# Kernel tuning notes

Measured on AMD Instinct MI355X. Metric: run time of the kernel, lower is better.

Reference implementation:

```python
import jax, jax.numpy as jnp
import numpy as np

N = 13627
E = 504378
D = 500


def _seg_softmax(e, seg, n):
    m = jax.ops.segment_max(e, seg, num_segments=n)
    ex = jnp.exp(e - m[seg])
    s = jax.ops.segment_sum(ex, seg, num_segments=n)
    return ex / (s[seg] + 1e-16)


def _gatv2(x, src, dst, Wl, Wr, att, b, n):
    # PyG GATv2Conv (heads=1): message = Wl x_src; score uses Wl x_src + Wr x_dst
    xl = x @ Wl                                   # [N, F]
    xr = x @ Wr                                   # [N, F]
    e = jax.nn.leaky_relu(xl[src] + xr[dst], 0.2) @ att   # [E]
    a = _seg_softmax(e, dst, n)                   # segment softmax over targets
    out = jax.ops.segment_sum(a[:, None] * xl[src], dst, num_segments=n)
    return out + b


def setup_inputs() -> dict:
    key = jax.random.key(0)
    ks = jax.random.split(key, 24)
    s = 0.05
    inp = {
        'x': jax.random.normal(ks[0], (N, D), dtype=jnp.float32),
        'edge_index': jax.random.randint(ks[1], (2, E), 0, N),
        'neg_edge_index': jax.random.randint(ks[2], (2, E), 0, N),
        'Wl1': jax.random.normal(ks[3], (D, 300)) * s,
        'Wr1': jax.random.normal(ks[4], (D, 300)) * s,
        'att1': jax.random.normal(ks[5], (300,)) * s,
        'b1': jnp.zeros((300,)),
        'Wl2': jax.random.normal(ks[6], (300, 100)) * s,
        'Wr2': jax.random.normal(ks[7], (300, 100)) * s,
        'att2': jax.random.normal(ks[8], (100,)) * s,
        'b2': jnp.zeros((100,)),
        'Wl3': jax.random.normal(ks[9], (100, 1)) * s,
        'Wr3': jax.random.normal(ks[10], (100, 1)) * s,
        'att3': jax.random.normal(ks[11], (1,)) * s,
        'b3': jnp.zeros((1,)),
        'W_lin1': jax.random.normal(ks[12], (D, 100)) * s,
        'b_lin1': jnp.zeros((100,)),
        'W_lin2': jax.random.normal(ks[13], (D, 100)) * s,
        'b_lin2': jnp.zeros((100,)),
        'c1': jnp.array([0.5], dtype=jnp.float32),
        'c2': jnp.array([0.5], dtype=jnp.float32),
    }
    return inp


def reference(x, edge_index, neg_edge_index, Wl1, Wr1, att1, b1, Wl2, Wr2, att2, b2,
              Wl3, Wr3, att3, b3, W_lin1, b_lin1, W_lin2, b_lin2, c1, c2):
    # eval mode: dropout / dropout_adj are identity
    loops = jnp.arange(N)
    src = jnp.concatenate([edge_index[0], loops])   # GATv2Conv adds self loops
    dst = jnp.concatenate([edge_index[1], loops])

    h1 = jax.nn.relu(_gatv2(x, src, dst, Wl1, Wr1, att1, b1, N))
    h2 = jax.nn.relu(_gatv2(h1, src, dst, Wl2, Wr2, att2, b2, N))

    xo = h2 + jax.nn.relu(x @ W_lin1 + b_lin1)
    z = h2 + jax.nn.relu(x @ W_lin2 + b_lin2)

    # link-prediction reconstruction loss
    pos_s = jnp.sum(z[edge_index[0]] * z[edge_index[1]], axis=1)
    pos_loss = -jnp.mean(jnp.log(jax.nn.sigmoid(pos_s) + 1e-15))
    neg_s = jnp.sum(z[neg_edge_index[0]] * z[neg_edge_index[1]], axis=1)
    neg_loss = -jnp.mean(jnp.log(1.0 - jax.nn.sigmoid(neg_s) + 1e-15))
    r_loss = pos_loss + neg_loss

    out = _gatv2(xo, src, dst, Wl3, Wr3, att3, b3, N)   # [N, 1]
    return out, r_loss, c1, c2
```

## Files before the change

kernel.cpp:

```cpp
#include <hip/hip_runtime.h>
#include <hip/hip_bf16.h>

#define NODES 13627
#define DIM   500

typedef short short8 __attribute__((ext_vector_type(8)));
typedef float f32x4 __attribute__((ext_vector_type(4)));
typedef float floatx2 __attribute__((ext_vector_type(2)));

__device__ inline float wave_reduce_sum(float v) {
#pragma unroll
    for (int o = 32; o > 0; o >>= 1) v += __shfl_xor(v, o, 64);
    return v;
}

__device__ inline void store_v(float* p, float v) { *p = v; }
__device__ inline void store_v(__hip_bfloat16* p, float v) { *p = __float2bfloat16(v); }

__device__ inline float blo(unsigned w) { unsigned t = w << 16;        return __builtin_bit_cast(float, t); }
__device__ inline float bhi(unsigned w) { unsigned t = w & 0xffff0000u; return __builtin_bit_cast(float, t); }

__device__ inline unsigned char to_fp8(float v) {
    int r = __builtin_amdgcn_cvt_pk_fp8_f32(v, v, 0, false);
    return (unsigned char)(r & 0xff);
}

__device__ inline unsigned pk2bf(float a, float b) {
    unsigned la = (unsigned)__builtin_bit_cast(unsigned short, __float2bfloat16(a));
    unsigned hb = (unsigned)__builtin_bit_cast(unsigned short, __float2bfloat16(b));
    return la | (hb << 16);
}

struct b4 { __hip_bfloat16 a, b, c, d; };

__global__ __launch_bounds__(256) void hist_kernel(const int* __restrict__ dst,
                                                   int* __restrict__ cnt, int E) {
    int i = blockIdx.x * blockDim.x + threadIdx.x;
    if (i < E) atomicAdd(&cnt[dst[i]], 1);
}

__global__ __launch_bounds__(1024) void scan_kernel(int* __restrict__ cnt_cur,
                                                    int* __restrict__ off, int n) {
    __shared__ int wsum[16];
    const int tid = threadIdx.x, lane = tid & 63, w = tid >> 6;
    int carry = 0;
    for (int base = 0; base < n; base += 1024) {
        int i = base + tid;
        int v = (i < n) ? cnt_cur[i] : 0;
        int s = v;
#pragma unroll
        for (int o = 1; o < 64; o <<= 1) {
            int t = __shfl_up(s, o, 64);
            if (lane >= o) s += t;
        }
        if (lane == 63) wsum[w] = s;
        __syncthreads();
        if (w == 0 && lane < 16) {
            int x = wsum[lane];
            int sx = x;
#pragma unroll
            for (int o = 1; o < 16; o <<= 1) {
                int t = __shfl_up(sx, o, 64);
                if (lane >= o) sx += t;
            }
            wsum[lane] = sx;
        }
        __syncthreads();
        int wo = (w == 0) ? 0 : wsum[w - 1];
        int total = wsum[15];
        int excl = carry + wo + (s - v);
        if (i < n) { off[i] = excl; cnt_cur[i] = excl; }
        carry += total;
        __syncthreads();
    }
    if (tid == 0) off[n] = carry;
}

__global__ __launch_bounds__(256) void scatter_kernel(const int* __restrict__ src,
                                                      const int* __restrict__ dst,
                                                      int* __restrict__ cur,
                                                      int* __restrict__ ssrc, int E) {
    int i = blockIdx.x * blockDim.x + threadIdx.x;
    if (i < E) {
        int p = atomicAdd(&cur[dst[i]], 1);
        ssrc[p] = src[i];
    }
}

__global__ __launch_bounds__(256) void convert_all_kernel(
    const float* __restrict__ x,
    const float* __restrict__ Wl1, const float* __restrict__ Wr1,
    const float* __restrict__ Wl2, const float* __restrict__ Wr2,
    const float* __restrict__ Ws1, const float* __restrict__ Ws2,
    const float* __restrict__ bs1, const float* __restrict__ bs2,
    __hip_bfloat16* __restrict__ W1T, __hip_bfloat16* __restrict__ W2T,
    __hip_bfloat16* __restrict__ WsT, float* __restrict__ bcat,
    __hip_bfloat16* __restrict__ xb, int M) {
    int i = blockIdx.x * 256 + threadIdx.x;
    if (i < 327680) {
        int n = i >> 9, k = i & 511;
        float v = 0.f;
        if (k < 500) {
            if (n < 300) v = Wl1[k * 300 + n];
            else if (n < 600) v = Wr1[k * 300 + n - 300];
        }
        W1T[i] = __float2bfloat16(v);
    } else if (i < 409600) {
        int j = i - 327680;
        int n = j / 320, k = j - n * 320;
        float v = 0.f;
        if (k < 300) {
            if (n < 100) v = Wl2[k * 100 + n];
            else if (n < 200) v = Wr2[k * 100 + n - 100];
        }
        W2T[j] = __float2bfloat16(v);
    } else if (i < 540672) {
        int j = i - 409600;
        int n = j >> 9, k = j & 511;
        float v = 0.f;
        if (k < 500) {
            if (n < 100) v = Ws1[k * 100 + n];
            else if (n < 200) v = Ws2[k * 100 + n - 100];
        }
        WsT[j] = __float2bfloat16(v);
    } else if (i < 540928) {
        int n = i - 540672;
        float v = 0.f;
        if (n < 100) v = bs1[n];
        else if (n < 200) v = bs2[n - 100];
        bcat[n] = v;
    } else {
        int j = i - 540928;
        if (j >= M * 128) return;
        int m = j >> 7, k = (j & 127) << 2;
        b4 o;
        if (k < 500) {
            float4 v = *(const float4*)(x + (size_t)m * 500 + k);
            o.a = __float2bfloat16(v.x); o.b = __float2bfloat16(v.y);
            o.c = __float2bfloat16(v.z); o.d = __float2bfloat16(v.w);
        } else {
            o.a = o.b = o.c = o.d = __float2bfloat16(0.f);
        }
        *(b4*)(xb + (size_t)m * 512 + k) = o;
    }
}

template <int EPI, typename TC>
__global__ __launch_bounds__(256) void mfma_gemm(
    const __hip_bfloat16* __restrict__ A, const __hip_bfloat16* __restrict__ BT,
    TC* __restrict__ C, const float* __restrict__ bias, const float* __restrict__ h2,
    unsigned char* __restrict__ p8, __hip_bfloat16* __restrict__ pb,
    int M, int Kp, int Nn, int ldc) {
    __shared__ short AsF[8 * 64 * 8];
    __shared__ short BsF[4 * 64 * 8];
    const int t = threadIdx.x;
    const int w = t >> 6, lane = t & 63;
    const int c = t & 3, rr = t >> 2;
    const int m0 = blockIdx.y * 128, n0 = blockIdx.x * 64;

    f32x4 acc[2][4];
#pragma unroll
    for (int i = 0; i < 2; i++)
#pragma unroll
        for (int j = 0; j < 4; j++) acc[i][j] = (f32x4){0.f, 0.f, 0.f, 0.f};

    for (int k0 = 0; k0 < Kp; k0 += 32) {
#pragma unroll
        for (int r = 0; r < 2; r++) {
            int m = r * 64 + rr;
            int gm = m0 + m; if (gm >= M) gm = M - 1;
            float4 v = *(const float4*)(A + (size_t)gm * Kp + k0 + c * 8);
            int mi = m >> 4, sl = m & 15;
            *(float4*)(&AsF[(mi * 64 + c * 16 + sl) * 8]) = v;
        }
        {
            int n = rr;
            float4 v = *(const float4*)(BT + (size_t)(n0 + n) * Kp + k0 + c * 8);
            int ni = n >> 4, sl = n & 15;
            *(float4*)(&BsF[(ni * 64 + c * 16 + sl) * 8]) = v;
        }
        __syncthreads();
        short8 a0 = *(const short8*)(&AsF[((w * 2 + 0) * 64 + lane) * 8]);
        short8 a1 = *(const short8*)(&AsF[((w * 2 + 1) * 64 + lane) * 8]);
#pragma unroll
        for (int j = 0; j < 4; j++) {
            short8 b = *(const short8*)(&BsF[(j * 64 + lane) * 8]);
            acc[0][j] = __builtin_amdgcn_mfma_f32_16x16x32_bf16(a0, b, acc[0][j], 0, 0, 0);
            acc[1][j] = __builtin_amdgcn_mfma_f32_16x16x32_bf16(a1, b, acc[1][j], 0, 0, 0);
        }
        __syncthreads();
    }

    const int q = lane >> 4, sl = lane & 15;
#pragma unroll
    for (int i = 0; i < 2; i++) {
#pragma unroll
        for (int j = 0; j < 4; j++) {
#pragma unroll
            for (int reg = 0; reg < 4; reg++) {
                int gm = m0 + w * 32 + i * 16 + q * 4 + reg;
                int gn = n0 + j * 16 + sl;
                if (gm >= M) continue;
                float v = acc[i][j][reg];
                if constexpr (EPI == 1) {
                    if (gn < 300)       p8[(size_t)gm * 304 + gn] = to_fp8(v);
                    else if (gn < 600)  pb[(size_t)gm * 320 + (gn - 300)] = __float2bfloat16(v);
                    else if (gn < 620)  pb[(size_t)gm * 320 + (gn - 300)] = __float2bfloat16(0.f);
                    else if (gn < 624)  p8[(size_t)gm * 304 + (gn - 320)] = 0;
                } else if constexpr (EPI == 2) {
                    if (gn < 100)       p8[(size_t)gm * 112 + gn] = to_fp8(v);
                    else if (gn < 200)  pb[(size_t)gm * 128 + (gn - 100)] = __float2bfloat16(v);
                    else if (gn < 212)  p8[(size_t)gm * 112 + (gn - 100)] = 0;
                    else if (gn < 240)  pb[(size_t)gm * 128 + (gn - 112)] = __float2bfloat16(0.f);
                } else if constexpr (EPI == 3) {
                    if (gn < 200) {
                        int cn = gn < 100 ? gn : gn - 100;
                        float val = fmaxf(v + bias[gn], 0.f) + h2[(size_t)gm * 100 + cn];
                        if (gn < 100) C[(size_t)gm * 100 + gn] = val;
                        else p8[(size_t)gm * 128 + (gn - 100)] = to_fp8(val);
                    } else if (gn < 228) {
                        p8[(size_t)gm * 128 + (gn - 100)] = 0;
                    }
                } else {
                    store_v(&C[(size_t)gm * ldc + gn], v);
                }
            }
        }
    }
}

template <int F, int NJ, int SL8, int SRB, int SOUT, int JSL, typename TOUT>
__global__ __launch_bounds__(256) void gat_f8_kernel(
    const unsigned char* __restrict__ xl8, const __hip_bfloat16* __restrict__ xrb,
    const float* __restrict__ att, const float* __restrict__ bias,
    const int* __restrict__ off, const int* __restrict__ ssrc,
    TOUT* __restrict__ out, int n) {
    __shared__ float sden[2];
    __shared__ float sacc[2][NJ * 64];
    const int t = threadIdx.x;
    const int lane = t & 63;
    const int sl = lane & 15, q = lane >> 4;
    const int half = (t >> 6) & 1;
    const int pairIdx = t >> 7;
    int wid = blockIdx.x * 2 + pairIdx;
    if (wid >= n) wid = n - 1;

    float attv[NJ * 4], xrv[NJ * 4], acc[NJ * 4];
    const unsigned* xru = (const unsigned*)xrb + (size_t)wid * (SRB / 2);
#pragma unroll
    for (int j = 0; j < NJ; j++) {
        const int f0 = sl * 4 + j * 64;
        if (f0 < F) {
            float4 a4 = *(const float4*)(att + f0);
            attv[j * 4 + 0] = a4.x; attv[j * 4 + 1] = a4.y;
            attv[j * 4 + 2] = a4.z; attv[j * 4 + 3] = a4.w;
        } else {
            attv[j * 4 + 0] = attv[j * 4 + 1] = attv[j * 4 + 2] = attv[j * 4 + 3] = 0.f;
        }
        unsigned u0 = __builtin_nontemporal_load(xru + (f0 >> 1));
        unsigned u1 = __builtin_nontemporal_load(xru + (f0 >> 1) + 1);
        xrv[j * 4 + 0] = blo(u0); xrv[j * 4 + 1] = bhi(u0);
        xrv[j * 4 + 2] = blo(u1); xrv[j * 4 + 3] = bhi(u1);
        acc[j * 4 + 0] = acc[j * 4 + 1] = acc[j * 4 + 2] = acc[j * 4 + 3] = 0.f;
    }

    const int s0 = off[wid], s1 = off[wid + 1];
    const int h0 = (s1 - s0) >> 1;
    const int eb = half ? (s0 + h0) : (s0 - 1);
    const int ee = half ? s1 : (s0 + h0);
    float den = 0.f;

    for (int e0 = eb; e0 < ee; e0 += 8) {
        const int eA = e0 + q, eB = e0 + 4 + q;
        const bool actA = eA < ee, actB = eB < ee;
        int srcA = wid, srcB = wid;
        if (actA && eA >= s0) srcA = __builtin_nontemporal_load(ssrc + eA);
        if (actB && eB >= s0) srcB = __builtin_nontemporal_load(ssrc + eB);
        const unsigned char* rowA = xl8 + (size_t)srcA * SL8;
        const unsigned char* rowB = xl8 + (size_t)srcB * SL8;
        unsigned uA[NJ], uB[NJ];
#pragma unroll
        for (int j = 0; j < NJ; j++) {
            const bool ld = (j < NJ - 1) || (sl < JSL);
            const int offb = sl * 4 + j * 64;
            uA[j] = ld ? *(const unsigned*)(rowA + offb) : 0u;
            uB[j] = ld ? *(const unsigned*)(rowB + offb) : 0u;
        }
        float xlvA[NJ * 4], xlvB[NJ * 4];
        float pA = 0.f, pB = 0.f;
#pragma unroll
        for (int j = 0; j < NJ; j++) {
            floatx2 loA = __builtin_amdgcn_cvt_pk_f32_fp8((int)uA[j], false);
            floatx2 hiA = __builtin_amdgcn_cvt_pk_f32_fp8((int)uA[j], true);
            floatx2 loB = __builtin_amdgcn_cvt_pk_f32_fp8((int)uB[j], false);
            floatx2 hiB = __builtin_amdgcn_cvt_pk_f32_fp8((int)uB[j], true);
            float vA[4] = {loA.x, loA.y, hiA.x, hiA.y};
            float vB[4] = {loB.x, loB.y, hiB.x, hiB.y};
#pragma unroll
            for (int cc = 0; cc < 4; cc++) {
                xlvA[j * 4 + cc] = vA[cc];
                xlvB[j * 4 + cc] = vB[cc];
                float tA = vA[cc] + xrv[j * 4 + cc];
                float tB = vB[cc] + xrv[j * 4 + cc];
                pA += attv[j * 4 + cc] * fmaxf(tA, 0.2f * tA);
                pB += attv[j * 4 + cc] * fmaxf(tB, 0.2f * tB);
            }
        }
        pA += __shfl_xor(pA, 1, 64);  pB += __shfl_xor(pB, 1, 64);
        pA += __shfl_xor(pA, 2, 64);  pB += __shfl_xor(pB, 2, 64);
        pA += __shfl_xor(pA, 4, 64);  pB += __shfl_xor(pB, 4, 64);
        pA += __shfl_xor(pA, 8, 64);  pB += __shfl_xor(pB, 8, 64);
        float exA = actA ? expf(pA) : 0.f;
        float exB = actB ? expf(pB) : 0.f;
        den += exA + exB;
#pragma unroll
        for (int i = 0; i < NJ * 4; i++) acc[i] += exA * xlvA[i] + exB * xlvB[i];
    }

#pragma unroll
    for (int o = 16; o <= 32; o <<= 1) {
        den += __shfl_xor(den, o, 64);
#pragma unroll
        for (int i = 0; i < NJ * 4; i++) acc[i] += __shfl_xor(acc[i], o, 64);
    }

    if (half == 1 && lane < 16) {
        if (lane == 0) sden[pairIdx] = den;
#pragma unroll
        for (int j = 0; j < NJ; j++)
            *(float4*)(&sacc[pairIdx][sl * 4 + j * 64]) =
                make_float4(acc[j * 4 + 0], acc[j * 4 + 1], acc[j * 4 + 2], acc[j * 4 + 3]);
    }
    __syncthreads();
    if (half == 0 && lane < 16) {
        den += sden[pairIdx];
        const float inv = 1.f / (den + 1e-16f);
#pragma unroll
        for (int j = 0; j < NJ; j++) {
            const int f0 = sl * 4 + j * 64;
            if (f0 >= SOUT) continue;
            float4 o4 = *(float4*)(&sacc[pairIdx][f0]);
            float vv[4] = {acc[j * 4 + 0] + o4.x, acc[j * 4 + 1] + o4.y,
                           acc[j * 4 + 2] + o4.z, acc[j * 4 + 3] + o4.w};
            float r[4];
#pragma unroll
            for (int cc = 0; cc < 4; cc++) {
                const int f = f0 + cc;
                float v = 0.f;
                if (f < F) v = fmaxf(vv[cc] * inv + bias[f], 0.f);
                r[cc] = v;
            }
            if constexpr (sizeof(TOUT) == 4) {
                float* op = (float*)out + (size_t)wid * SOUT + f0;
                __builtin_nontemporal_store(r[0], op + 0);
                __builtin_nontemporal_store(r[1], op + 1);
                __builtin_nontemporal_store(r[2], op + 2);
                __builtin_nontemporal_store(r[3], op + 3);
            } else {
                unsigned* op = (unsigned*)out + (size_t)wid * (SOUT / 2) + (f0 >> 1);
                __builtin_nontemporal_store(pk2bf(r[0], r[1]), op);
                __builtin_nontemporal_store(pk2bf(r[2], r[3]), op + 1);
            }
        }
    }
}

__global__ __launch_bounds__(256) void gemm_vec1_kernel(
    const float* __restrict__ xo, const float* __restrict__ wl,
    const float* __restrict__ wr, float* __restrict__ xl3,
    float* __restrict__ xr3, int M, int ldx) {
    const int wid = blockIdx.x * 4 + (threadIdx.x >> 6);
    const int lane = threadIdx.x & 63;
    if (wid >= M) return;
    float a = 0.f, b = 0.f;
    for (int f = lane; f < 100; f += 64) {
        float v = xo[(size_t)wid * ldx + f];
        a += v * wl[f];
        b += v * wr[f];
    }
    a = wave_reduce_sum(a);
    b = wave_reduce_sum(b);
    if (lane == 0) { xl3[wid] = a; xr3[wid] = b; }
}

__global__ __launch_bounds__(256) void gat3_kernel(
    const float* __restrict__ xl3, const float* __restrict__ xr3,
    const float* __restrict__ att3, const float* __restrict__ b3,
    const int* __restrict__ off, const int* __restrict__ ssrc,
    float* __restrict__ out, int n) {
    const int wid = blockIdx.x * 4 + (threadIdx.x >> 6);
    const int lane = threadIdx.x & 63;
    if (wid >= n) return;
    const float xrv = xr3[wid];
    const float att = att3[0];
    float num = 0.f, den = 0.f;
    const int s0 = off[wid], s1 = off[wid + 1];
    for (int e = s0 - 1 + lane; e < s1; e += 64) {
        int src = (e < s0) ? wid : ssrc[e];
        float xlv = xl3[src];
        float t = xlv + xrv;
        float g = t > 0.f ? t : 0.2f * t;
        float ex = expf(g * att);
        den += ex;
        num += ex * xlv;
    }
    num = wave_reduce_sum(num);
    den = wave_reduce_sum(den);
    if (lane == 0) out[wid] = num / (den + 1e-16f) + b3[0];
}

__global__ __launch_bounds__(256) void loss_kernel(
    const unsigned char* __restrict__ z8, const int* __restrict__ pos,
    const int* __restrict__ neg, float* __restrict__ part, int nb, int E) {
    const int lane = threadIdx.x & 63;
    const int sl = lane & 15;
    const int wlocal = threadIdx.x >> 6;
    const int q = lane >> 4;
    const int nq = gridDim.x * 16;
    const int qid = (blockIdx.x * 4 + wlocal) * 4 + q;
    const int total = 2 * E;
    float psum = 0.f, nsum = 0.f;

    for (int base = qid; base < total; base += 4 * nq) {
        uint2 au[4], bu[4];
        bool act[4], isN[4];
#pragma unroll
        for (int s = 0; s < 4; s++) {
            int it = base + s * nq;
            act[s] = it < total;
            int itc = act[s] ? it : 0;
            isN[s] = itc >= E;
            int e = isN[s] ? itc - E : itc;
            const int* ei = isN[s] ? neg : pos;
            int u = ei[e], v = ei[E + e];
            au[s] = *(const uint2*)(z8 + (size_t)u * 128 + sl * 8);
            bu[s] = *(const uint2*)(z8 + (size_t)v * 128 + sl * 8);
        }
#pragma unroll
        for (int s = 0; s < 4; s++) {
            floatx2 a0 = __builtin_amdgcn_cvt_pk_f32_fp8((int)au[s].x, false);
            floatx2 a1 = __builtin_amdgcn_cvt_pk_f32_fp8((int)au[s].x, true);
            floatx2 a2 = __builtin_amdgcn_cvt_pk_f32_fp8((int)au[s].y, false);
            floatx2 a3 = __builtin_amdgcn_cvt_pk_f32_fp8((int)au[s].y, true);
            floatx2 b0 = __builtin_amdgcn_cvt_pk_f32_fp8((int)bu[s].x, false);
            floatx2 b1 = __builtin_amdgcn_cvt_pk_f32_fp8((int)bu[s].x, true);
            floatx2 b2 = __builtin_amdgcn_cvt_pk_f32_fp8((int)bu[s].y, false);
            floatx2 b3 = __builtin_amdgcn_cvt_pk_f32_fp8((int)bu[s].y, true);
            float p = a0.x * b0.x + a0.y * b0.y + a1.x * b1.x + a1.y * b1.y
                    + a2.x * b2.x + a2.y * b2.y + a3.x * b3.x + a3.y * b3.y;
            p += __shfl_xor(p, 1, 64);
            p += __shfl_xor(p, 2, 64);
            p += __shfl_xor(p, 4, 64);
            p += __shfl_xor(p, 8, 64);
            if (sl == 0 && act[s]) {
                float sig = 1.f / (1.f + expf(-p));
                if (isN[s]) nsum += logf(1.f - sig + 1e-15f);
                else        psum += logf(sig + 1e-15f);
            }
        }
    }
    float pw = wave_reduce_sum(psum);
    float nw = wave_reduce_sum(nsum);
    __shared__ float sp[4], sn[4];
    if (lane == 0) { sp[wlocal] = pw; sn[wlocal] = nw; }
    __syncthreads();
    if (threadIdx.x == 0) {
        part[blockIdx.x]      = sp[0] + sp[1] + sp[2] + sp[3];
        part[nb + blockIdx.x] = sn[0] + sn[1] + sn[2] + sn[3];
    }
}

__global__ __launch_bounds__(1024) void finalize_kernel(
    const float* __restrict__ part, int nb,
    const float* __restrict__ c1, const float* __restrict__ c2,
    float* __restrict__ out, int n, int E) {
    __shared__ float sp[16], sn[16];
    const int tid = threadIdx.x, lane = tid & 63, w = tid >> 6;
    float p = 0.f, q = 0.f;
    for (int i = tid; i < nb; i += 1024) { p += part[i]; q += part[nb + i]; }
    p = wave_reduce_sum(p);
    q = wave_reduce_sum(q);
    if (lane == 0) { sp[w] = p; sn[w] = q; }
    __syncthreads();
    if (tid == 0) {
        float tp = 0.f, tq = 0.f;
#pragma unroll
        for (int i = 0; i < 16; i++) { tp += sp[i]; tq += sn[i]; }
        out[n]     = -(tp + tq) / (float)E;
        out[n + 1] = c1[0];
        out[n + 2] = c2[0];
    }
}

extern "C" void kernel_launch(void* const* d_in, const int* in_sizes, int n_in,
                              void* d_out, int out_size, void* d_ws, size_t ws_size,
                              hipStream_t stream) {
    const float* x      = (const float*)d_in[0];
    const int*   ei     = (const int*)d_in[1];
    const int*   nei    = (const int*)d_in[2];
    const float* Wl1    = (const float*)d_in[3];
    const float* Wr1    = (const float*)d_in[4];
    const float* att1   = (const float*)d_in[5];
    const float* b1     = (const float*)d_in[6];
    const float* Wl2    = (const float*)d_in[7];
    const float* Wr2    = (const float*)d_in[8];
    const float* att2   = (const float*)d_in[9];
    const float* b2     = (const float*)d_in[10];
    const float* Wl3    = (const float*)d_in[11];
    const float* Wr3    = (const float*)d_in[12];
    const float* att3   = (const float*)d_in[13];
    const float* b3     = (const float*)d_in[14];
    const float* Wlin1  = (const float*)d_in[15];
    const float* blin1  = (const float*)d_in[16];
    const float* Wlin2  = (const float*)d_in[17];
    const float* blin2  = (const float*)d_in[18];
    const float* c1     = (const float*)d_in[19];
    const float* c2     = (const float*)d_in[20];
    float* out = (float*)d_out;

    const int E = in_sizes[1] / 2;
    const int N = NODES;
    const int LOSS_BLOCKS = 4096;

    char* ws = (char*)d_ws;
    unsigned char*  xl8  = (unsigned char*)(ws + 0);
    unsigned char*  xl28 = (unsigned char*)(ws + 0);
    __hip_bfloat16* xrb  = (__hip_bfloat16*)(ws + 4194304);
    __hip_bfloat16* xr2b = (__hip_bfloat16*)(ws + 4194304);
    float*          xo   = (float*)(ws + 4194304);
    unsigned char*  z8   = (unsigned char*)(ws + 9645312);
    __hip_bfloat16* h1b  = (__hip_bfloat16*)(ws + 12915712);
    float*          h2   = (float*)(ws + 12915712);
    __hip_bfloat16* xb   = (__hip_bfloat16*)(ws + 21637120);
    __hip_bfloat16* W1T  = (__hip_bfloat16*)(ws + 35591168);
    __hip_bfloat16* W2T  = (__hip_bfloat16*)(ws + 36246528);
    __hip_bfloat16* WsT  = (__hip_bfloat16*)(ws + 36410368);
    float*          bcat = (float*)(ws + 36672512);
    float*          xl3  = (float*)(ws + 36673536);
    float*          xr3  = (float*)(ws + 36728064);
    int*            ioff = (int*)(ws + 36782592);
    int*            cur  = (int*)(ws + 36837376);
    int*            ssrc = (int*)(ws + 36892160);
    float*          part = (float*)(ws + 38909952);

    hipMemsetAsync(cur, 0, sizeof(int) * N, stream);

    hist_kernel<<<(E + 255) / 256, 256, 0, stream>>>(ei + E, cur, E);
    scan_kernel<<<1, 1024, 0, stream>>>(cur, ioff, N);
    scatter_kernel<<<(E + 255) / 256, 256, 0, stream>>>(ei, ei + E, cur, ssrc, E);

    convert_all_kernel<<<(540928 + N * 128 + 255) / 256, 256, 0, stream>>>(
        x, Wl1, Wr1, Wl2, Wr2, Wlin1, Wlin2, blin1, blin2,
        W1T, W2T, WsT, bcat, xb, N);

    mfma_gemm<1, __hip_bfloat16><<<dim3(10, 107), 256, 0, stream>>>(
        xb, W1T, (__hip_bfloat16*)nullptr, nullptr, nullptr, xl8, xrb, N, 512, 640, 0);
    gat_f8_kernel<300, 5, 304, 320, 320, 11, __hip_bfloat16>
        <<<(N + 1) / 2, 256, 0, stream>>>(xl8, xrb, att1, b1, ioff, ssrc, h1b, N);

    mfma_gemm<2, __hip_bfloat16><<<dim3(4, 107), 256, 0, stream>>>(
        h1b, W2T, (__hip_bfloat16*)nullptr, nullptr, nullptr, xl28, xr2b, N, 320, 256, 0);
    gat_f8_kernel<100, 2, 112, 128, 100, 9, float>
        <<<(N + 1) / 2, 256, 0, stream>>>(xl28, xr2b, att2, b2, ioff, ssrc, h2, N);

    mfma_gemm<3, float><<<dim3(4, 107), 256, 0, stream>>>(
        xb, WsT, xo, bcat, h2, z8, nullptr, N, 512, 256, 0);

    loss_kernel<<<LOSS_BLOCKS, 256, 0, stream>>>(z8, ei, nei, part, LOSS_BLOCKS, E);

    gemm_vec1_kernel<<<(N + 3) / 4, 256, 0, stream>>>(xo, Wl3, Wr3, xl3, xr3, N, 100);
    gat3_kernel<<<(N + 3) / 4, 256, 0, stream>>>(xl3, xr3, att3, b3, ioff, ssrc, out, N);

    finalize_kernel<<<1, 1024, 0, stream>>>(part, LOSS_BLOCKS, c1, c2, out, N, E);
}
```

Baseline: 403.4 us.

## Decompose leaky-ReLU attention score into per-node dots plus abs term

Rewrites leaky_relu(s) as 0.6*s + 0.4*|s|, so the linear part of the attention score becomes per-node dot products att·xl and att·xr. A new kernel precomputes these once per node, leaving only an fma with fabs per feature in the edge loop. The GAT edge loop also drops from two edges per iteration to one, which lowers register pressure at the cost of less memory-level parallelism per iteration. It adds an extra kernel launch and small per-node arrays, and the algebraic split slightly changes floating-point rounding.

After: 408.3 us. About the same (+1.2%).

```diff
diff --git a/kernel.cpp b/kernel.cpp
--- a/kernel.cpp
+++ b/kernel.cpp
@@ -229,10 +229,34 @@
     }
 }
 
+template <int F, int SL8, int SRB>
+__global__ __launch_bounds__(256) void attdot_kernel(
+    const unsigned char* __restrict__ xl8, const __hip_bfloat16* __restrict__ xrb,
+    const float* __restrict__ att, float* __restrict__ sxl, float* __restrict__ sxr,
+    int n) {
+    const int wid = blockIdx.x * 4 + (threadIdx.x >> 6);
+    const int lane = threadIdx.x & 63;
+    if (wid >= n) return;
+    float al = 0.f, ar = 0.f;
+    for (int f0 = lane * 4; f0 < F; f0 += 256) {
+        float4 a = *(const float4*)(att + f0);
+        unsigned u = *(const unsigned*)(xl8 + (size_t)wid * SL8 + f0);
+        floatx2 lo = __builtin_amdgcn_cvt_pk_f32_fp8((int)u, false);
+        floatx2 hi = __builtin_amdgcn_cvt_pk_f32_fp8((int)u, true);
+        al += a.x * lo.x + a.y * lo.y + a.z * hi.x + a.w * hi.y;
+        uint2 r = *(const uint2*)(xrb + (size_t)wid * SRB + f0);
+        ar += a.x * blo(r.x) + a.y * bhi(r.x) + a.z * blo(r.y) + a.w * bhi(r.y);
+    }
+    al = wave_reduce_sum(al);
+    ar = wave_reduce_sum(ar);
+    if (lane == 0) { sxl[wid] = 0.6f * al; sxr[wid] = 0.6f * ar; }
+}
+
 template <int F, int NJ, int SL8, int SRB, int SOUT, int JSL, typename TOUT>
 __global__ __launch_bounds__(256) void gat_f8_kernel(
     const unsigned char* __restrict__ xl8, const __hip_bfloat16* __restrict__ xrb,
     const float* __restrict__ att, const float* __restrict__ bias,
+    const float* __restrict__ sxl, const float* __restrict__ sxr,
     const int* __restrict__ off, const int* __restrict__ ssrc,
     TOUT* __restrict__ out, int n) {
     __shared__ float sden[2];
@@ -245,17 +269,17 @@
     int wid = blockIdx.x * 2 + pairIdx;
     if (wid >= n) wid = n - 1;
 
-    float attv[NJ * 4], xrv[NJ * 4], acc[NJ * 4];
+    float att4[NJ * 4], xrv[NJ * 4], acc[NJ * 4];
     const unsigned* xru = (const unsigned*)xrb + (size_t)wid * (SRB / 2);
 #pragma unroll
     for (int j = 0; j < NJ; j++) {
         const int f0 = sl * 4 + j * 64;
         if (f0 < F) {
             float4 a4 = *(const float4*)(att + f0);
-            attv[j * 4 + 0] = a4.x; attv[j * 4 + 1] = a4.y;
-            attv[j * 4 + 2] = a4.z; attv[j * 4 + 3] = a4.w;
+            att4[j * 4 + 0] = 0.4f * a4.x; att4[j * 4 + 1] = 0.4f * a4.y;
+            att4[j * 4 + 2] = 0.4f * a4.z; att4[j * 4 + 3] = 0.4f * a4.w;
         } else {
-            attv[j * 4 + 0] = attv[j * 4 + 1] = attv[j * 4 + 2] = attv[j * 4 + 3] = 0.f;
+            att4[j * 4 + 0] = att4[j * 4 + 1] = att4[j * 4 + 2] = att4[j * 4 + 3] = 0.f;
         }
         unsigned u0 = __builtin_nontemporal_load(xru + (f0 >> 1));
         unsigned u1 = __builtin_nontemporal_load(xru + (f0 >> 1) + 1);
@@ -263,6 +287,7 @@
         xrv[j * 4 + 2] = blo(u1); xrv[j * 4 + 3] = bhi(u1);
         acc[j * 4 + 0] = acc[j * 4 + 1] = acc[j * 4 + 2] = acc[j * 4 + 3] = 0.f;
     }
+    const float pbase = sxr[wid];
 
     const int s0 = off[wid], s1 = off[wid + 1];
     const int h0 = (s1 - s0) >> 1;
@@ -270,51 +295,40 @@
     const int ee = half ? s1 : (s0 + h0);
     float den = 0.f;
 
-    for (int e0 = eb; e0 < ee; e0 += 8) {
-        const int eA = e0 + q, eB = e0 + 4 + q;
-        const bool actA = eA < ee, actB = eB < ee;
-        int srcA = wid, srcB = wid;
-        if (actA && eA >= s0) srcA = __builtin_nontemporal_load(ssrc + eA);
-        if (actB && eB >= s0) srcB = __builtin_nontemporal_load(ssrc + eB);
-        const unsigned char* rowA = xl8 + (size_t)srcA * SL8;
-        const unsigned char* rowB = xl8 + (size_t)srcB * SL8;
-        unsigned uA[NJ], uB[NJ];
+    for (int e0 = eb; e0 < ee; e0 += 4) {
+        const int eq = e0 + q;
+        const bool act = eq < ee;
+        int src = wid;
+        if (act && eq >= s0) src = __builtin_nontemporal_load(ssrc + eq);
+        const unsigned char* row = xl8 + (size_t)src * SL8;
+        unsigned u[NJ];
 #pragma unroll
         for (int j = 0; j < NJ; j++) {
             const bool ld = (j < NJ - 1) || (sl < JSL);
-            const int offb = sl * 4 + j * 64;
-            uA[j] = ld ? *(const unsigned*)(rowA + offb) : 0u;
-            uB[j] = ld ? *(const unsigned*)(rowB + offb) : 0u;
-        }
-        float xlvA[NJ * 4], xlvB[NJ * 4];
-        float pA = 0.f, pB = 0.f;
+            u[j] = ld ? *(const unsigned*)(row + sl * 4 + j * 64) : 0u;
+        }
+        float xlv[NJ * 4];
+        float p = (sl == 0) ? (pbase + sxl[src]) : 0.f;
 #pragma unroll
         for (int j = 0; j < NJ; j++) {
-            floatx2 loA = __builtin_amdgcn_cvt_pk_f32_fp8((int)uA[j], false);
-            floatx2 hiA = __builtin_amdgcn_cvt_pk_f32_fp8((int)uA[j], true);
-            floatx2 loB = __builtin_amdgcn_cvt_pk_f32_fp8((int)uB[j], false);
-            floatx2 hiB = __builtin_amdgcn_cvt_pk_f32_fp8((int)uB[j], true);
-            float vA[4] = {loA.x, loA.y, hiA.x, hiA.y};
-            float vB[4] = {loB.x, loB.y, hiB.x, hiB.y};
+            floatx2 lo = __builtin_amdgcn_cvt_pk_f32_fp8((int)u[j], false);
+            floatx2 hi = __builtin_amdgcn_cvt_pk_f32_fp8((int)u[j], true);
+            float v[4] = {lo.x, lo.y, hi.x, hi.y};
 #pragma unroll
             for (int cc = 0; cc < 4; cc++) {
-                xlvA[j * 4 + cc] = vA[cc];
-                xlvB[j * 4 + cc] = vB[cc];
-                float tA = vA[cc] + xrv[j * 4 + cc];
-                float tB = vB[cc] + xrv[j * 4 + cc];
-                pA += attv[j * 4 + cc] * fmaxf(tA, 0.2f * tA);
-                pB += attv[j * 4 + cc] * fmaxf(tB, 0.2f * tB);
+                xlv[j * 4 + cc] = v[cc];
+                float s = v[cc] + xrv[j * 4 + cc];
+                p = fmaf(att4[j * 4 + cc], fabsf(s), p);
             }
         }
-        pA += __shfl_xor(pA, 1, 64);  pB += __shfl_xor(pB, 1, 64);
-        pA += __shfl_xor(pA, 2, 64);  pB += __shfl_xor(pB, 2, 64);
-        pA += __shfl_xor(pA, 4, 64);  pB += __shfl_xor(pB, 4, 64);
-        pA += __shfl_xor(pA, 8, 64);  pB += __shfl_xor(pB, 8, 64);
-        float exA = actA ? expf(pA) : 0.f;
-        float exB = actB ? expf(pB) : 0.f;
-        den += exA + exB;
-#pragma unroll
-        for (int i = 0; i < NJ * 4; i++) acc[i] += exA * xlvA[i] + exB * xlvB[i];
+        p += __shfl_xor(p, 1, 64);
+        p += __shfl_xor(p, 2, 64);
+        p += __shfl_xor(p, 4, 64);
+        p += __shfl_xor(p, 8, 64);
+        float ex = act ? expf(p) : 0.f;
+        den += ex;
+#pragma unroll
+        for (int i = 0; i < NJ * 4; i++) acc[i] += ex * xlv[i];
     }
 
 #pragma unroll
@@ -542,6 +556,8 @@
     int*            cur  = (int*)(ws + 36837376);
     int*            ssrc = (int*)(ws + 36892160);
     float*          part = (float*)(ws + 38909952);
+    float*          sxl  = (float*)(ws + 38942720);
+    float*          sxr  = (float*)(ws + 38997248);
 
     hipMemsetAsync(cur, 0, sizeof(int) * N, stream);
 
@@ -555,13 +571,17 @@
 
     mfma_gemm<1, __hip_bfloat16><<<dim3(10, 107), 256, 0, stream>>>(
         xb, W1T, (__hip_bfloat16*)nullptr, nullptr, nullptr, xl8, xrb, N, 512, 640, 0);
+    attdot_kernel<300, 304, 320><<<(N + 3) / 4, 256, 0, stream>>>(
+        xl8, xrb, att1, sxl, sxr, N);
     gat_f8_kernel<300, 5, 304, 320, 320, 11, __hip_bfloat16>
-        <<<(N + 1) / 2, 256, 0, stream>>>(xl8, xrb, att1, b1, ioff, ssrc, h1b, N);
+        <<<(N + 1) / 2, 256, 0, stream>>>(xl8, xrb, att1, b1, sxl, sxr, ioff, ssrc, h1b, N);
 
     mfma_gemm<2, __hip_bfloat16><<<dim3(4, 107), 256, 0, stream>>>(
         h1b, W2T, (__hip_bfloat16*)nullptr, nullptr, nullptr, xl28, xr2b, N, 320, 256, 0);
+    attdot_kernel<100, 112, 128><<<(N + 3) / 4, 256, 0, stream>>>(
+        xl28, xr2b, att2, sxl, sxr, N);
     gat_f8_kernel<100, 2, 112, 128, 100, 9, float>
-        <<<(N + 1) / 2, 256, 0, stream>>>(xl28, xr2b, att2, b2, ioff, ssrc, h2, N);
+        <<<(N + 1) / 2, 256, 0, stream>>>(xl28, xr2b, att2, b2, sxl, sxr, ioff, ssrc, h2, N);
 
     mfma_gemm<3, float><<<dim3(4, 107), 256, 0, stream>>>(
         xb, WsT, xo, bcat, h2, z8, nullptr, N, 512, 256, 0);
```
